# Kernel optimization log

Hardware: AMD Instinct MI355X
Metric: run time of the kernel (lower is better)

The kernel has to match this reference:

```python
import jax, jax.numpy as jnp
import numpy as np

D = 256      # d_model
NH = 8       # num heads
L = 2        # encoder layers
FF = 512     # dim_feedforward
WS = 2       # HiLo window_size
HD = D // NH # head dim = 32
LH = 4       # lofi heads (alpha=0.5)
HH = 4       # hifi heads
LD = LH * HD # 128
HDIM = HH * HD  # 128
SCALE = HD ** -0.5


def _ln(x, g, b):
    m = jnp.mean(x, -1, keepdims=True)
    v = jnp.mean((x - m) ** 2, -1, keepdims=True)
    return (x - m) / jnp.sqrt(v + 1e-5) * g + b


def _hilo(x, H, Wlq, Wlkv, Wlp, blp, Whqkv, Whp, bhp):
    N, B, C = x.shape
    x = x.reshape(B, H, N // H, C)  # faithful to torch: pure reshape, no permute
    Bc, Hh, Ww, Cc = x.shape
    hg, wg = Hh // WS, Ww // WS
    tg, n = hg * wg, WS * WS
    # ---- hifi: local windowed attention ----
    xg = x.reshape(Bc, hg, WS, wg, WS, Cc).swapaxes(2, 3).reshape(Bc, tg, n, Cc)
    qkv = (xg @ Whqkv).reshape(Bc, tg, n, 3, HH, HD)
    qkv = jnp.transpose(qkv, (3, 0, 1, 4, 2, 5))  # (3, B, tg, heads, n, hd)
    q, k, v = qkv[0], qkv[1], qkv[2]
    a = jax.nn.softmax((q @ jnp.swapaxes(k, -2, -1)) * SCALE, axis=-1)
    o = (a @ v).swapaxes(2, 3).reshape(Bc, hg, wg, WS, WS, HDIM)
    o = o.swapaxes(2, 3).reshape(Bc, Hh, Ww, HDIM)
    hi = o @ Whp + bhp
    # ---- lofi: full queries vs avg-pooled kv ----
    q = (x @ Wlq).reshape(Bc, Hh * Ww, LH, HD).transpose(0, 2, 1, 3)
    xp = x.reshape(Bc, hg, WS, wg, WS, Cc).mean(axis=(2, 4)).reshape(Bc, tg, Cc)
    kv = (xp @ Wlkv).reshape(Bc, tg, 2, LH, HD).transpose(2, 0, 3, 1, 4)
    k, v = kv[0], kv[1]
    a = jax.nn.softmax((q @ jnp.swapaxes(k, -2, -1)) * SCALE, axis=-1)
    lo = (a @ v).swapaxes(1, 2).reshape(Bc, Hh, Ww, LD) @ Wlp + blp
    return jnp.concatenate([hi, lo], axis=-1).reshape(N, B, C)


def setup_inputs() -> dict:
    key = jax.random.key(0)
    ks = jax.random.split(key, 10)
    w = lambda k, s: jax.random.normal(k, s, jnp.float32) * 0.02
    N, B = 128, 1024
    return {
        "tgt": jax.random.normal(ks[0], (N, B, D), jnp.float32),
        "Wlq": w(ks[1], (L, D, LD)),
        "Wlkv": w(ks[2], (L, D, 2 * LD)),
        "Wlp": w(ks[3], (L, LD, LD)),
        "blp": jnp.zeros((L, LD), jnp.float32),
        "Whqkv": w(ks[4], (L, D, 3 * HDIM)),
        "Whp": w(ks[5], (L, HDIM, HDIM)),
        "bhp": jnp.zeros((L, HDIM), jnp.float32),
        "W1": w(ks[6], (L, D, FF)),
        "b1": jnp.zeros((L, FF), jnp.float32),
        "W2": w(ks[7], (L, FF, D)),
        "b2": jnp.zeros((L, D), jnp.float32),
        "ln1_g": jnp.ones((L, D), jnp.float32),
        "ln1_b": jnp.zeros((L, D), jnp.float32),
        "ln2_g": jnp.ones((L, D), jnp.float32),
        "ln2_b": jnp.zeros((L, D), jnp.float32),
        "lnf_g": jnp.ones((D,), jnp.float32),
        "lnf_b": jnp.zeros((D,), jnp.float32),
        "enc_win_h": 8,
    }


def reference(tgt, Wlq, Wlkv, Wlp, blp, Whqkv, Whp, bhp, W1, b1, W2, b2,
              ln1_g, ln1_b, ln2_g, ln2_b, lnf_g, lnf_b, enc_win_h):
    out = tgt
    for i in range(L):
        a = _hilo(out, enc_win_h, Wlq[i], Wlkv[i], Wlp[i], blp[i], Whqkv[i], Whp[i], bhp[i])
        out = _ln(out + a, ln1_g[i], ln1_b[i])
        f = jax.nn.relu(out @ W1[i] + b1[i]) @ W2[i] + b2[i]
        out = _ln(out + f, ln2_g[i], ln2_b[i])
    out = _ln(out, lnf_g, lnf_b)
    return out[None]  # (1, N, B, C), matching output.unsqueeze(0)
```

## Files before the change

### kernel.cpp

```cpp
#include <hip/hip_runtime.h>
#include <hip/hip_bf16.h>


#define RT 131072ull
#define ATT_SCALE 0.17677669529663687f

typedef float f32x4 __attribute__((ext_vector_type(4)));
typedef __bf16 bf16x8 __attribute__((ext_vector_type(8)));
typedef unsigned short u16x8 __attribute__((ext_vector_type(8)));
typedef unsigned short u16x4 __attribute__((ext_vector_type(4)));

__device__ __forceinline__ unsigned short f2bf(float f) {
    unsigned int u = __float_as_uint(f);
    return (unsigned short)((u + 0x7FFFu + ((u >> 16) & 1u)) >> 16);
}
__device__ __forceinline__ float bf2f(unsigned short s) {
    return __uint_as_float(((unsigned int)s) << 16);
}

__global__ __launch_bounds__(256) void wprep(const float* __restrict__ src,
                                             unsigned short* __restrict__ dst,
                                             int K, int N)
{
    __shared__ unsigned short t[32][33];
    int l = blockIdx.z;
    const float* s = src + (size_t)l * K * N;
    unsigned short* d = dst + (size_t)l * K * N;
    int r = threadIdx.x >> 3, c4 = (threadIdx.x & 7) * 4;
    int kb = blockIdx.x * 32, nb = blockIdx.y * 32;
    f32x4 v = *(const f32x4*)(s + (size_t)(kb + r) * N + nb + c4);
    #pragma unroll
    for (int j = 0; j < 4; ++j) t[c4 + j][r] = f2bf(v[j]);
    __syncthreads();
    u16x4 o;
    #pragma unroll
    for (int j = 0; j < 4; ++j) o[j] = t[r][c4 + j];
    *(u16x4*)(d + (size_t)(nb + r) * K + kb + c4) = o;
}

__global__ __launch_bounds__(256) void cvt_bf16(const float* __restrict__ src,
                                                unsigned short* __restrict__ dst)
{
    size_t i = ((size_t)blockIdx.x * 256 + threadIdx.x) * 8;
    f32x4 a = *(const f32x4*)(src + i);
    f32x4 b = *(const f32x4*)(src + i + 4);
    u16x8 t;
    #pragma unroll
    for (int j = 0; j < 4; ++j) { t[j] = f2bf(a[j]); t[4 + j] = f2bf(b[j]); }
    *(u16x8*)(dst + i) = t;
}

template<int BN, bool BIAS, bool RELU>
__global__ __launch_bounds__(256) void gemm_bb(
    const unsigned short* __restrict__ A, int lda,
    const unsigned short* __restrict__ BT,
    const float* __restrict__ bias,
    unsigned short* __restrict__ C, int ldc, int K)
{
    constexpr int NT = BN / 32;
    __shared__ __align__(16) char As[128 * 128];
    __shared__ __align__(16) char Bs[BN * 128];

    const int tid = threadIdx.x;
    const int hw = blockIdx.x + gridDim.x * blockIdx.y;
    const int nwg = gridDim.x * gridDim.y;
    const int logical = (hw & 7) * (nwg >> 3) + (hw >> 3);
    const int n0 = (logical % gridDim.x) * BN;
    const size_t m0 = (size_t)(logical / gridDim.x) * 128;

    const int w = tid >> 6, l = tid & 63;
    const int lr = l & 15, lk = l >> 4;
    const int wm = w >> 1, wn = w & 1;

    f32x4 acc[4][NT] = {};

    for (int k0 = 0; k0 < K; k0 += 64) {
        #pragma unroll
        for (int i = 0; i < 4; ++i) {
            int cid = tid + i * 256, row = cid >> 3, kc = cid & 7;
            u16x8 t = *(const u16x8*)(A + (m0 + row) * lda + k0 + kc * 8);
            *(u16x8*)(As + ((row * 128 + kc * 16) ^ ((row & 7) << 4))) = t;
        }
        #pragma unroll
        for (int i = 0; i < BN / 32; ++i) {
            int fid = tid + i * 256, row = fid >> 3, kc = fid & 7;
            u16x8 t = *(const u16x8*)(BT + (size_t)(n0 + row) * K + k0 + kc * 8);
            *(u16x8*)(Bs + ((row * 128 + kc * 16) ^ ((row & 7) << 4))) = t;
        }
        __syncthreads();
        #pragma unroll
        for (int s = 0; s < 2; ++s) {
            bf16x8 bfr[NT];
            #pragma unroll
            for (int nt = 0; nt < NT; ++nt) {
                int r = wn * (BN / 2) + nt * 16 + lr;
                bfr[nt] = *(const bf16x8*)(Bs + ((r * 128 + s * 64 + lk * 16) ^ ((r & 7) << 4)));
            }
            #pragma unroll
            for (int mt = 0; mt < 4; ++mt) {
                int r = wm * 64 + mt * 16 + lr;
                bf16x8 afr = *(const bf16x8*)(As + ((r * 128 + s * 64 + lk * 16) ^ ((r & 7) << 4)));
                #pragma unroll
                for (int nt = 0; nt < NT; ++nt)
                    acc[mt][nt] = __builtin_amdgcn_mfma_f32_16x16x32_bf16(afr, bfr[nt], acc[mt][nt], 0, 0, 0);
            }
        }
        __syncthreads();
    }
    #pragma unroll
    for (int nt = 0; nt < NT; ++nt) {
        int col = n0 + wn * (BN / 2) + nt * 16 + lr;
        float bv = BIAS ? bias[col] : 0.0f;
        #pragma unroll
        for (int mt = 0; mt < 4; ++mt) {
            #pragma unroll
            for (int j = 0; j < 4; ++j) {
                size_t row = m0 + (size_t)(wm * 64 + mt * 16 + lk * 4 + j);
                float v = acc[mt][nt][j] + bv;
                if (RELU) v = fmaxf(v, 0.0f);
                C[row * ldc + col] = f2bf(v);
            }
        }
    }
}

__global__ __launch_bounds__(256) void hifi_attn(const unsigned short* __restrict__ qkv,
                                                 unsigned short* __restrict__ os)
{
    int t = blockIdx.x * 256 + threadIdx.x;
    int wdw = t >> 4, h = (t >> 2) & 3, qi = t & 3;
    int bc = wdw >> 5, tw = wdw & 31;
    int rbase = bc * 128 + (tw >> 3) * 32 + (tw & 7) * 2;
    int qrow = rbase + ((qi >> 1) << 4) + (qi & 1);

    const unsigned short* qp = qkv + (size_t)qrow * 384 + h * 32;
    float q[32];
    #pragma unroll
    for (int c = 0; c < 4; ++c) {
        u16x8 v = *(const u16x8*)(qp + c * 8);
        #pragma unroll
        for (int j = 0; j < 8; ++j) q[c * 8 + j] = bf2f(v[j]);
    }
    float s4[4];
    #pragma unroll
    for (int j = 0; j < 4; ++j) {
        int kr = rbase + ((j >> 1) << 4) + (j & 1);
        const unsigned short* kp = qkv + (size_t)kr * 384 + 128 + h * 32;
        float d = 0.0f;
        #pragma unroll
        for (int c = 0; c < 4; ++c) {
            u16x8 v = *(const u16x8*)(kp + c * 8);
            #pragma unroll
            for (int jj = 0; jj < 8; ++jj) d += q[c * 8 + jj] * bf2f(v[jj]);
        }
        s4[j] = d * ATT_SCALE;
    }
    float mx = fmaxf(fmaxf(s4[0], s4[1]), fmaxf(s4[2], s4[3]));
    float den = 0.0f;
    #pragma unroll
    for (int j = 0; j < 4; ++j) { s4[j] = __expf(s4[j] - mx); den += s4[j]; }
    float inv = 1.0f / den;

    float o[32];
    #pragma unroll
    for (int i = 0; i < 32; ++i) o[i] = 0.0f;
    #pragma unroll
    for (int j = 0; j < 4; ++j) {
        int vr = rbase + ((j >> 1) << 4) + (j & 1);
        const unsigned short* vp = qkv + (size_t)vr * 384 + 256 + h * 32;
        float a = s4[j] * inv;
        #pragma unroll
        for (int c = 0; c < 4; ++c) {
            u16x8 v = *(const u16x8*)(vp + c * 8);
            #pragma unroll
            for (int jj = 0; jj < 8; ++jj) o[c * 8 + jj] += a * bf2f(v[jj]);
        }
    }
    unsigned short* op = os + (size_t)qrow * 128 + h * 32;
    #pragma unroll
    for (int c = 0; c < 4; ++c) {
        u16x8 v;
        #pragma unroll
        for (int j = 0; j < 8; ++j) v[j] = f2bf(o[c * 8 + j]);
        *(u16x8*)(op + c * 8) = v;
    }
}

__global__ __launch_bounds__(256) void pool_k(const unsigned short* __restrict__ x,
                                              unsigned short* __restrict__ xp)
{
    int id = blockIdx.x * 256 + threadIdx.x;
    int p = id >> 5, c8 = (id & 31) * 8;
    int bc = p >> 5, tw = p & 31;
    int rbase = bc * 128 + (tw >> 3) * 32 + (tw & 7) * 2;
    const unsigned short* x0 = x + (size_t)rbase * 256 + c8;
    float a[8] = {};
    const int offs[4] = {0, 256, 16 * 256, 17 * 256};
    #pragma unroll
    for (int r = 0; r < 4; ++r) {
        u16x8 v = *(const u16x8*)(x0 + offs[r]);
        #pragma unroll
        for (int j = 0; j < 8; ++j) a[j] += bf2f(v[j]);
    }
    u16x8 o;
    #pragma unroll
    for (int j = 0; j < 8; ++j) o[j] = f2bf(a[j] * 0.25f);
    *(u16x8*)(xp + (size_t)p * 256 + c8) = o;
}

__global__ __launch_bounds__(128) void lofi_attn(const unsigned short* __restrict__ qb,
                                                 const unsigned short* __restrict__ kvb,
                                                 unsigned short* __restrict__ ob)
{
    __shared__ float ks[32][36];
    __shared__ float vs[32][36];
    int bc = blockIdx.x >> 2, h = blockIdx.x & 3;
    int tid = threadIdx.x;

    #pragma unroll
    for (int i = 0; i < 2; ++i) {
        int fid = tid + i * 128;
        int row = fid >> 3, cc = (fid & 7) * 4;
        const unsigned short* kp = kvb + (size_t)(bc * 32 + row) * 256 + h * 32 + cc;
        u16x4 kk = *(const u16x4*)kp;
        u16x4 vv = *(const u16x4*)(kp + 128);
        #pragma unroll
        for (int j = 0; j < 4; ++j) { ks[row][cc + j] = bf2f(kk[j]); vs[row][cc + j] = bf2f(vv[j]); }
    }

    const unsigned short* qp = qb + (size_t)(bc * 128 + tid) * 128 + h * 32;
    float q[32];
    #pragma unroll
    for (int c = 0; c < 4; ++c) {
        u16x8 v = *(const u16x8*)(qp + c * 8);
        #pragma unroll
        for (int j = 0; j < 8; ++j) q[c * 8 + j] = bf2f(v[j]);
    }
    __syncthreads();

    float sc[32];
    #pragma unroll
    for (int tk = 0; tk < 32; ++tk) {
        float d = 0.0f;
        #pragma unroll
        for (int i = 0; i < 32; ++i) d += q[i] * ks[tk][i];
        sc[tk] = d * ATT_SCALE;
    }
    float mx = -1e30f;
    #pragma unroll
    for (int tk = 0; tk < 32; ++tk) mx = fmaxf(mx, sc[tk]);
    float den = 0.0f;
    #pragma unroll
    for (int tk = 0; tk < 32; ++tk) { sc[tk] = __expf(sc[tk] - mx); den += sc[tk]; }
    float inv = 1.0f / den;

    float o[32];
    #pragma unroll
    for (int i = 0; i < 32; ++i) o[i] = 0.0f;
    #pragma unroll
    for (int tk = 0; tk < 32; ++tk) {
        float a = sc[tk];
        #pragma unroll
        for (int i = 0; i < 32; ++i) o[i] += a * vs[tk][i];
    }
    unsigned short* op = ob + (size_t)(bc * 128 + tid) * 128 + h * 32;
    #pragma unroll
    for (int c = 0; c < 4; ++c) {
        u16x8 v;
        #pragma unroll
        for (int j = 0; j < 8; ++j) v[j] = f2bf(o[c * 8 + j] * inv);
        *(u16x8*)(op + c * 8) = v;
    }
}

template<int MODE>
__global__ __launch_bounds__(256) void addln(
    const unsigned short* __restrict__ x,
    const unsigned short* __restrict__ r1,
    const unsigned short* __restrict__ r2,
    const float* __restrict__ g, const float* __restrict__ b,
    const float* __restrict__ g2, const float* __restrict__ b2,
    unsigned short* __restrict__ xout, float* __restrict__ fout)
{
    size_t row = (size_t)blockIdx.x * 4 + (threadIdx.x >> 6);
    int l = threadIdx.x & 63;
    u16x4 xv = *(const u16x4*)(x + row * 256 + l * 4);
    f32x4 v;
    #pragma unroll
    for (int j = 0; j < 4; ++j) v[j] = bf2f(xv[j]);
    if (MODE == 0) {
        const unsigned short* rp = (l < 32) ? (r1 + row * 128 + l * 4)
                                            : (r2 + row * 128 + (l - 32) * 4);
        u16x4 rv = *(const u16x4*)rp;
        #pragma unroll
        for (int j = 0; j < 4; ++j) v[j] += bf2f(rv[j]);
    } else {
        u16x4 rv = *(const u16x4*)(r1 + row * 256 + l * 4);
        #pragma unroll
        for (int j = 0; j < 4; ++j) v[j] += bf2f(rv[j]);
    }
    float s = v[0] + v[1] + v[2] + v[3];
    float sq = v[0] * v[0] + v[1] * v[1] + v[2] * v[2] + v[3] * v[3];
    #pragma unroll
    for (int off = 32; off > 0; off >>= 1) { s += __shfl_xor(s, off); sq += __shfl_xor(sq, off); }
    float mean = s * (1.0f / 256.0f);
    float rstd = rsqrtf(sq * (1.0f / 256.0f) - mean * mean + 1e-5f);
    f32x4 gv = *(const f32x4*)(g + l * 4);
    f32x4 bv = *(const f32x4*)(b + l * 4);
    f32x4 o;
    #pragma unroll
    for (int j = 0; j < 4; ++j) o[j] = (v[j] - mean) * rstd * gv[j] + bv[j];
    if (MODE == 2) {
        float s2 = o[0] + o[1] + o[2] + o[3];
        float sq2 = o[0] * o[0] + o[1] * o[1] + o[2] * o[2] + o[3] * o[3];
        #pragma unroll
        for (int off = 32; off > 0; off >>= 1) { s2 += __shfl_xor(s2, off); sq2 += __shfl_xor(sq2, off); }
        float mean2 = s2 * (1.0f / 256.0f);
        float rstd2 = rsqrtf(sq2 * (1.0f / 256.0f) - mean2 * mean2 + 1e-5f);
        f32x4 g2v = *(const f32x4*)(g2 + l * 4);
        f32x4 b2v = *(const f32x4*)(b2 + l * 4);
        f32x4 f;
        #pragma unroll
        for (int j = 0; j < 4; ++j) f[j] = (o[j] - mean2) * rstd2 * g2v[j] + b2v[j];
        *(f32x4*)(fout + row * 256 + l * 4) = f;
    } else {
        u16x4 t;
        #pragma unroll
        for (int j = 0; j < 4; ++j) t[j] = f2bf(o[j]);
        *(u16x4*)(xout + row * 256 + l * 4) = t;
    }
}

extern "C" void kernel_launch(void* const* d_in, const int* in_sizes, int n_in,
                              void* d_out, int out_size, void* d_ws, size_t ws_size,
                              hipStream_t stream)
{
    (void)in_sizes; (void)n_in; (void)out_size; (void)ws_size;
    const float* tgt   = (const float*)d_in[0];
    const float* Wlq   = (const float*)d_in[1];
    const float* Wlkv  = (const float*)d_in[2];
    const float* Wlp   = (const float*)d_in[3];
    const float* blp   = (const float*)d_in[4];
    const float* Whqkv = (const float*)d_in[5];
    const float* Whp   = (const float*)d_in[6];
    const float* bhp   = (const float*)d_in[7];
    const float* W1    = (const float*)d_in[8];
    const float* b1    = (const float*)d_in[9];
    const float* W2    = (const float*)d_in[10];
    const float* b2    = (const float*)d_in[11];
    const float* ln1g  = (const float*)d_in[12];
    const float* ln1b  = (const float*)d_in[13];
    const float* ln2g  = (const float*)d_in[14];
    const float* ln2b  = (const float*)d_in[15];
    const float* lnfg  = (const float*)d_in[16];
    const float* lnfb  = (const float*)d_in[17];

    unsigned short* wsu = (unsigned short*)d_ws;
    unsigned short* tWhqkv = wsu;
    unsigned short* tWhp   = wsu + 196608;
    unsigned short* tWlq   = wsu + 229376;
    unsigned short* tWlkv  = wsu + 294912;
    unsigned short* tWlp   = wsu + 425984;
    unsigned short* tW1    = wsu + 458752;
    unsigned short* tW2    = wsu + 720896;
    unsigned short* x    = wsu + 983040;
    unsigned short* qkv  = x + RT * 256;
    unsigned short* f    = qkv;
    unsigned short* los  = qkv + RT * 256;
    unsigned short* os   = qkv + RT * 384;
    unsigned short* qb   = os;
    unsigned short* xp   = os + RT * 128;
    unsigned short* kv   = xp + 32768ull * 256;
    unsigned short* hi   = kv + 32768ull * 256;
    unsigned short* lo   = hi + RT * 128;
    unsigned short* hbuf = hi;

    wprep<<<dim3(8, 12, 2), 256, 0, stream>>>(Whqkv, tWhqkv, 256, 384);
    wprep<<<dim3(4,  4, 2), 256, 0, stream>>>(Whp,   tWhp,   128, 128);
    wprep<<<dim3(8,  4, 2), 256, 0, stream>>>(Wlq,   tWlq,   256, 128);
    wprep<<<dim3(8,  8, 2), 256, 0, stream>>>(Wlkv,  tWlkv,  256, 256);
    wprep<<<dim3(4,  4, 2), 256, 0, stream>>>(Wlp,   tWlp,   128, 128);
    wprep<<<dim3(8, 16, 2), 256, 0, stream>>>(W1,    tW1,    256, 512);
    wprep<<<dim3(16, 8, 2), 256, 0, stream>>>(W2,    tW2,    512, 256);

    cvt_bf16<<<16384, 256, 0, stream>>>(tgt, x);

    for (int li = 0; li < 2; ++li) {
        gemm_bb<128, false, false><<<dim3(3, 1024), 256, 0, stream>>>(
            x, 256, tWhqkv + (size_t)li * 98304, nullptr, qkv, 384, 256);
        hifi_attn<<<2048, 256, 0, stream>>>(qkv, os);
        gemm_bb<128, true, false><<<dim3(1, 1024), 256, 0, stream>>>(
            os, 128, tWhp + (size_t)li * 16384, bhp + li * 128, hi, 128, 128);
        gemm_bb<128, false, false><<<dim3(1, 1024), 256, 0, stream>>>(
            x, 256, tWlq + (size_t)li * 32768, nullptr, qb, 128, 256);
        pool_k<<<4096, 256, 0, stream>>>(x, xp);
        gemm_bb<128, false, false><<<dim3(2, 256), 256, 0, stream>>>(
            xp, 256, tWlkv + (size_t)li * 65536, nullptr, kv, 256, 256);
        lofi_attn<<<4096, 128, 0, stream>>>(qb, kv, los);
        gemm_bb<128, true, false><<<dim3(1, 1024), 256, 0, stream>>>(
            los, 128, tWlp + (size_t)li * 16384, blp + li * 128, lo, 128, 128);
        addln<0><<<32768, 256, 0, stream>>>(x, hi, lo, ln1g + li * 256, ln1b + li * 256,
                                            nullptr, nullptr, x, nullptr);
        gemm_bb<128, true, true><<<dim3(4, 1024), 256, 0, stream>>>(
            x, 256, tW1 + (size_t)li * 131072, b1 + li * 512, hbuf, 512, 256);
        gemm_bb<128, true, false><<<dim3(2, 1024), 256, 0, stream>>>(
            hbuf, 512, tW2 + (size_t)li * 131072, b2 + li * 256, f, 256, 512);
        if (li == 0) {
            addln<1><<<32768, 256, 0, stream>>>(x, f, nullptr, ln2g, ln2b,
                                                nullptr, nullptr, x, nullptr);
        } else {
            addln<2><<<32768, 256, 0, stream>>>(x, f, nullptr, ln2g + 256, ln2b + 256,
                                                lnfg, lnfb, nullptr, (float*)d_out);
        }
    }
}
```

Measured before the change: 892.0 us.

## Register-prefetch GEMM tiles and merge hifi/lofi projection GEMMs into one launch

The GEMM body now loads the next K-tile from global memory into registers while MFMAs run on the current shared-memory tile, so global load latency overlaps with compute. The two 128x128 output projections (hifi Whp and lofi Wlp) are combined into one grouped kernel launch over 2048 blocks, which removes one launch and its tail. The lofi query buffer also reuses hbuf in place of qb. The prefetch costs extra registers, which may lower occupancy.

```diff
diff --git a/kernel.cpp b/kernel.cpp
--- a/kernel.cpp
+++ b/kernel.cpp
@@ -51,43 +51,57 @@
 }
 
 template<int BN, bool BIAS, bool RELU>
-__global__ __launch_bounds__(256) void gemm_bb(
-    const unsigned short* __restrict__ A, int lda,
-    const unsigned short* __restrict__ BT,
+__device__ __forceinline__ void gemm_body(
+    const unsigned short* __restrict__ A, int lda, size_t m0,
+    const unsigned short* __restrict__ BT, int n0,
     const float* __restrict__ bias,
     unsigned short* __restrict__ C, int ldc, int K)
 {
     constexpr int NT = BN / 32;
+    constexpr int BCH = BN / 32;
     __shared__ __align__(16) char As[128 * 128];
     __shared__ __align__(16) char Bs[BN * 128];
 
     const int tid = threadIdx.x;
-    const int hw = blockIdx.x + gridDim.x * blockIdx.y;
-    const int nwg = gridDim.x * gridDim.y;
-    const int logical = (hw & 7) * (nwg >> 3) + (hw >> 3);
-    const int n0 = (logical % gridDim.x) * BN;
-    const size_t m0 = (size_t)(logical / gridDim.x) * 128;
-
     const int w = tid >> 6, l = tid & 63;
     const int lr = l & 15, lk = l >> 4;
     const int wm = w >> 1, wn = w & 1;
 
     f32x4 acc[4][NT] = {};
 
-    for (int k0 = 0; k0 < K; k0 += 64) {
+    u16x8 ra[4], rb[BCH];
+
+    auto gload = [&](int k0) {
         #pragma unroll
         for (int i = 0; i < 4; ++i) {
             int cid = tid + i * 256, row = cid >> 3, kc = cid & 7;
-            u16x8 t = *(const u16x8*)(A + (m0 + row) * lda + k0 + kc * 8);
-            *(u16x8*)(As + ((row * 128 + kc * 16) ^ ((row & 7) << 4))) = t;
-        }
-        #pragma unroll
-        for (int i = 0; i < BN / 32; ++i) {
+            ra[i] = *(const u16x8*)(A + (m0 + row) * lda + k0 + kc * 8);
+        }
+        #pragma unroll
+        for (int i = 0; i < BCH; ++i) {
             int fid = tid + i * 256, row = fid >> 3, kc = fid & 7;
-            u16x8 t = *(const u16x8*)(BT + (size_t)(n0 + row) * K + k0 + kc * 8);
-            *(u16x8*)(Bs + ((row * 128 + kc * 16) ^ ((row & 7) << 4))) = t;
-        }
+            rb[i] = *(const u16x8*)(BT + (size_t)(n0 + row) * K + k0 + kc * 8);
+        }
+    };
+    auto lstore = [&]() {
+        #pragma unroll
+        for (int i = 0; i < 4; ++i) {
+            int cid = tid + i * 256, row = cid >> 3, kc = cid & 7;
+            *(u16x8*)(As + ((row * 128 + kc * 16) ^ ((row & 7) << 4))) = ra[i];
+        }
+        #pragma unroll
+        for (int i = 0; i < BCH; ++i) {
+            int fid = tid + i * 256, row = fid >> 3, kc = fid & 7;
+            *(u16x8*)(Bs + ((row * 128 + kc * 16) ^ ((row & 7) << 4))) = rb[i];
+        }
+    };
+
+    const int nk = K >> 6;
+    gload(0);
+    for (int t = 0; t < nk; ++t) {
+        lstore();
         __syncthreads();
+        if (t + 1 < nk) gload((t + 1) << 6);
         #pragma unroll
         for (int s = 0; s < 2; ++s) {
             bf16x8 bfr[NT];
@@ -122,6 +136,45 @@
             }
         }
     }
+}
+
+template<int BN, bool BIAS, bool RELU>
+__global__ __launch_bounds__(256) void gemm_bb(
+    const unsigned short* __restrict__ A, int lda,
+    const unsigned short* __restrict__ BT,
+    const float* __restrict__ bias,
+    unsigned short* __restrict__ C, int ldc, int K)
+{
+    const int hw = blockIdx.x + gridDim.x * blockIdx.y;
+    const int nwg = gridDim.x * gridDim.y;
+    const int logical = (hw & 7) * (nwg >> 3) + (hw >> 3);
+    const int n0 = (logical % gridDim.x) * BN;
+    const size_t m0 = (size_t)(logical / gridDim.x) * 128;
+    gemm_body<BN, BIAS, RELU>(A, lda, m0, BT, n0, bias, C, ldc, K);
+}
+
+__global__ __launch_bounds__(256) void gemm_hilo(
+    const unsigned short* __restrict__ os,
+    const unsigned short* __restrict__ los,
+    const unsigned short* __restrict__ tWhp,
+    const unsigned short* __restrict__ tWlp,
+    const float* __restrict__ bhp, const float* __restrict__ blp,
+    unsigned short* __restrict__ hi, unsigned short* __restrict__ lo)
+{
+    const int hw = blockIdx.x + gridDim.x * blockIdx.y;
+    const int nwg = gridDim.x * gridDim.y;
+    const int logical = (hw & 7) * (nwg >> 3) + (hw >> 3);
+    size_t mp = (size_t)logical;
+    const unsigned short* A;
+    const unsigned short* BT;
+    const float* bias;
+    unsigned short* C;
+    if (mp < 1024) {
+        A = os;  BT = tWhp; bias = bhp; C = hi;
+    } else {
+        A = los; BT = tWlp; bias = blp; C = lo; mp -= 1024;
+    }
+    gemm_body<128, true, false>(A, 128, mp * 128, BT, 0, bias, C, 128, 128);
 }
 
 __global__ __launch_bounds__(256) void hifi_attn(const unsigned short* __restrict__ qkv,
@@ -389,16 +442,15 @@
         gemm_bb<128, false, false><<<dim3(3, 1024), 256, 0, stream>>>(
             x, 256, tWhqkv + (size_t)li * 98304, nullptr, qkv, 384, 256);
         hifi_attn<<<2048, 256, 0, stream>>>(qkv, os);
-        gemm_bb<128, true, false><<<dim3(1, 1024), 256, 0, stream>>>(
-            os, 128, tWhp + (size_t)li * 16384, bhp + li * 128, hi, 128, 128);
         gemm_bb<128, false, false><<<dim3(1, 1024), 256, 0, stream>>>(
-            x, 256, tWlq + (size_t)li * 32768, nullptr, qb, 128, 256);
+            x, 256, tWlq + (size_t)li * 32768, nullptr, hbuf, 128, 256);
         pool_k<<<4096, 256, 0, stream>>>(x, xp);
         gemm_bb<128, false, false><<<dim3(2, 256), 256, 0, stream>>>(
             xp, 256, tWlkv + (size_t)li * 65536, nullptr, kv, 256, 256);
-        lofi_attn<<<4096, 128, 0, stream>>>(qb, kv, los);
-        gemm_bb<128, true, false><<<dim3(1, 1024), 256, 0, stream>>>(
-            los, 128, tWlp + (size_t)li * 16384, blp + li * 128, lo, 128, 128);
+        lofi_attn<<<4096, 128, 0, stream>>>(hbuf, kv, los);
+        gemm_hilo<<<dim3(1, 2048), 256, 0, stream>>>(
+            os, los, tWhp + (size_t)li * 16384, tWlp + (size_t)li * 16384,
+            bhp + li * 128, blp + li * 128, hi, lo);
         addln<0><<<32768, 256, 0, stream>>>(x, hi, lo, ln1g + li * 256, ln1b + li * 256,
                                             nullptr, nullptr, x, nullptr);
         gemm_bb<128, true, true><<<dim3(4, 1024), 256, 0, stream>>>(
```

New measurement: 829.4 us. 1.08x faster.
